# Kernel optimization log

Hardware: AMD Instinct MI355X
Metric: run time of the kernel (lower is better)

Reference implementation:

```python
import jax, jax.numpy as jnp
import numpy as np

B, T, N, D, H, C = 32, 64, 22, 512, 8, 128
DEPTH = D // H


def setup_inputs() -> dict:
    key = jax.random.key(0)
    ks = jax.random.split(key, 10)
    s = 0.02
    return {
        "x": jax.random.normal(ks[0], (B, T, N, D), jnp.float32),
        "context": jax.random.normal(ks[1], (B, C, D), jnp.float32),
        "Wq": jax.random.normal(ks[2], (N, D, D), jnp.float32) * s,  # per-joint Q proj
        "bq": jax.random.normal(ks[3], (N, D), jnp.float32) * s,
        "Wk": jax.random.normal(ks[4], (D, D), jnp.float32) * s,
        "bk": jax.random.normal(ks[5], (D,), jnp.float32) * s,
        "Wv": jax.random.normal(ks[6], (D, D), jnp.float32) * s,
        "bv": jax.random.normal(ks[7], (D,), jnp.float32) * s,
        "Wout": jax.random.normal(ks[8], (D, D), jnp.float32) * s,
        "bout": jax.random.normal(ks[9], (D,), jnp.float32) * s,
    }


def reference(x, context, Wq, bq, Wk, bk, Wv, bv, Wout, bout):
    b, t, n, d = x.shape
    c = context.shape[1]
    h, dh = H, DEPTH
    # Per-joint Q projection fused into one batched GEMM: [B,T,N,D] x [N,D,D] -> [B,T,N,D]
    q = jnp.einsum('btnd,ndf->btnf', x, Wq) + bq  # bq broadcasts over (B,T)
    # Shared K/V computed ONCE (original recomputes per joint; math identical)
    k = context @ Wk + bk  # [B,C,D]
    v = context @ Wv + bv  # [B,C,D]
    # Split heads
    qh = q.reshape(b, t, n, h, dh)
    kh = k.reshape(b, c, h, dh)
    vh = v.reshape(b, c, h, dh)
    scale = 1.0 / float(np.sqrt(dh))
    # Attention logits per joint: [B,N,H,T,C]
    logits = jnp.einsum('btnhd,bchd->bnhtc', qh, kh) * scale
    attn = jax.nn.softmax(logits, axis=-1)
    # Attend shared V, merge heads: [B,T,N,D]
    o = jnp.einsum('bnhtc,bchd->btnhd', attn, vh).reshape(b, t, n, d)
    # Shared output projection
    return o @ Wout + bout
```

## Files before the change

### kernel.cpp

```cpp
#include <hip/hip_runtime.h>
#include <hip/hip_bf16.h>

#define NB 32
#define NT 64
#define NJ 22
#define ND 512
#define NH 8
#define NC 128
#define NDH 64
#define NR 1408

typedef __attribute__((ext_vector_type(8))) short s16x8;
typedef __attribute__((ext_vector_type(4))) float fx4;

static __device__ __forceinline__ unsigned short f2bf(float f) {
    unsigned u = __builtin_bit_cast(unsigned, f);
    u += 0x7fffu + ((u >> 16) & 1u);
    return (unsigned short)(u >> 16);
}

static __device__ __forceinline__ fx4 mfma16(s16x8 a, s16x8 b, fx4 c) {
    return __builtin_amdgcn_mfma_f32_16x16x32_bf16(a, b, c, 0, 0, 0);
}

static __device__ __forceinline__ void gload16(const void* g, void* l) {
    __builtin_amdgcn_global_load_lds(
        (const __attribute__((address_space(1))) void*)g,
        (__attribute__((address_space(3))) void*)l,
        16, 0, 0);
}

__global__ __launch_bounds__(256) void convswz_all_k(
    const float* __restrict__ x, const float* __restrict__ ctx,
    unsigned short* __restrict__ xbf, unsigned short* __restrict__ cbf)
{
    const long bid = blockIdx.x;
    const float* src; unsigned short* dst; long i; int key;
    if (bid < 11264) {
        i = (bid * 256 + threadIdx.x) * 8;
        src = x; dst = xbf;
        key = (int)(((unsigned)(i >> 9) / 22u) & 7u);
    } else {
        i = ((bid - 11264) * 256 + threadIdx.x) * 8;
        src = ctx; dst = cbf;
        key = (int)(((unsigned)(i >> 9)) & 7u);
    }
    const int c = (int)((i >> 3) & 7);
    const long j = (i & ~63L) | ((long)(c ^ key) << 3);
    const float4 a = *reinterpret_cast<const float4*>(src + i);
    const float4 b = *reinterpret_cast<const float4*>(src + i + 4);
    unsigned short t[8];
    t[0]=f2bf(a.x); t[1]=f2bf(a.y); t[2]=f2bf(a.z); t[3]=f2bf(a.w);
    t[4]=f2bf(b.x); t[5]=f2bf(b.y); t[6]=f2bf(b.z); t[7]=f2bf(b.w);
    *reinterpret_cast<s16x8*>(dst + j) = *reinterpret_cast<s16x8*>(t);
}

__global__ __launch_bounds__(256) void twconv_all_k(
    const float* __restrict__ Wq, const float* __restrict__ Wk,
    const float* __restrict__ Wv, const float* __restrict__ Wout,
    unsigned short* __restrict__ WqT, unsigned short* __restrict__ WkT,
    unsigned short* __restrict__ WvT, unsigned short* __restrict__ WoutT)
{
    __shared__ float T[64][65];
    const int z = blockIdx.z;
    const float* W; unsigned short* Wt;
    if (z < 22)       { W = Wq + (long)z * 262144; Wt = WqT + (long)z * 262144; }
    else if (z == 22) { W = Wk;   Wt = WkT; }
    else if (z == 23) { W = Wv;   Wt = WvT; }
    else              { W = Wout; Wt = WoutT; }

    const int tid = threadIdx.x;
    W  += (long)blockIdx.x * 64 * 512 + blockIdx.y * 64;
    Wt += (long)blockIdx.y * 64 * 512 + blockIdx.x * 64;
    const int r = tid >> 2, c0 = (tid & 3) * 16;
    #pragma unroll
    for (int i = 0; i < 4; ++i) {
        const float4 p = *reinterpret_cast<const float4*>(W + (long)r * 512 + c0 + i*4);
        T[r][c0 + i*4 + 0] = p.x; T[r][c0 + i*4 + 1] = p.y;
        T[r][c0 + i*4 + 2] = p.z; T[r][c0 + i*4 + 3] = p.w;
    }
    __syncthreads();
    unsigned short o[16];
    #pragma unroll
    for (int i = 0; i < 16; ++i) o[i] = f2bf(T[c0 + i][r]);
    const int ch0 = ((c0 >> 3) ^ (r & 7));
    *reinterpret_cast<s16x8*>(Wt + (long)r * 512 + ch0*8)     = *reinterpret_cast<s16x8*>(o);
    *reinterpret_cast<s16x8*>(Wt + (long)r * 512 + (ch0^1)*8) = *reinterpret_cast<s16x8*>(o + 8);
}

template <typename TC, int MODE>
__global__ __launch_bounds__(256) void gemm128_k(
    const unsigned short* __restrict__ A, long lda,
    const unsigned short* __restrict__ Bt,
    const float* __restrict__ bias,
    TC* __restrict__ C, long ldc,
    long jsA, long jsW, long jsB, long jsC,
    const unsigned short* __restrict__ Bt2,
    const float* __restrict__ bias2,
    TC* __restrict__ C2)
{
    __shared__ unsigned short As[2][128*64];
    __shared__ unsigned short Bs[2][128*64];

    const int tid = threadIdx.x;
    const int w = tid >> 6, lane = tid & 63;
    const long j = blockIdx.z;

    const int nx = gridDim.x;
    const int nwg = nx * gridDim.y;
    int lin = blockIdx.y * nx + blockIdx.x;
    lin = (lin & 7) * (nwg >> 3) + (lin >> 3);
    const int bx = lin % nx, by = lin / nx;

    int kv = 0;
    int byv = by;
    if constexpr (MODE == 3) {
        if (by >= 4) { kv = 2; byv = by - 4; Bt = Bt2; bias = bias2; C = C2; }
        else         { kv = 1; }
    }

    A    += (long)bx * 128 * lda + j * jsA;
    Bt   += j * jsW + (long)byv * 128 * 512;
    bias += j * jsB + byv * 128;
    if constexpr (MODE == 0)
        C += (long)bx * 128 * ldc + j * jsC + byv * 128;

    const int srow = lane >> 3;
    const int scol = (lane & 7) * 8;
    const unsigned short* Ag = A  + (long)(w*8 + srow) * lda + scol;
    const unsigned short* Bg = Bt + (long)(w*8 + srow) * 512 + scol;

    const int lr = lane & 15, lk = lane >> 4;
    const int wm = w >> 1, wn = w & 1;

    fx4 acc[4][4] = {};

    auto STAGE = [&](int buf, int kt) {
        char* Al = (char*)&As[buf][0] + w * 1024;
        char* Bl = (char*)&Bs[buf][0] + w * 1024;
        #pragma unroll
        for (int it = 0; it < 4; ++it)
            gload16(Ag + (long)it * 32 * lda + kt, Al + it * 4096);
        #pragma unroll
        for (int it = 0; it < 4; ++it)
            gload16(Bg + (long)it * 32 * 512 + kt, Bl + it * 4096);
    };

    auto COMPUTE = [&](int buf) {
        #pragma unroll
        for (int ks = 0; ks < 2; ++ks) {
            const int cha = (ks*4 + lk) ^ (lr & 7);
            s16x8 a[4], b[4];
            #pragma unroll
            for (int m = 0; m < 4; ++m)
                a[m] = *reinterpret_cast<const s16x8*>(&As[buf][(wm*64 + m*16 + lr)*64 + cha*8]);
            #pragma unroll
            for (int n = 0; n < 4; ++n)
                b[n] = *reinterpret_cast<const s16x8*>(&Bs[buf][(wn*64 + n*16 + lr)*64 + cha*8]);
            #pragma unroll
            for (int m = 0; m < 4; ++m)
                #pragma unroll
                for (int n = 0; n < 4; ++n)
                    acc[m][n] = mfma16(a[m], b[n], acc[m][n]);
        }
    };

    STAGE(0, 0);
    __syncthreads();
    #pragma unroll
    for (int t = 0; t < 7; ++t) {
        const int cur = t & 1;
        STAGE(cur ^ 1, (t + 1) * 64);
        COMPUTE(cur);
        __syncthreads();
    }
    COMPUTE(1);

    #pragma unroll
    for (int n = 0; n < 4; ++n) {
        const int col = wn*64 + n*16 + lr;
        const float bv = bias[col];
        #pragma unroll
        for (int m = 0; m < 4; ++m) {
            #pragma unroll
            for (int r = 0; r < 4; ++r) {
                const int row = wm*64 + m*16 + lk*4 + r;
                const float val = acc[m][n][r] + bv;
                if constexpr (MODE == 0) {
                    if constexpr (sizeof(TC) == 2)
                        reinterpret_cast<unsigned short*>(C)[(long)row*ldc + col] = f2bf(val);
                    else
                        reinterpret_cast<float*>(C)[(long)row*ldc + col] = val;
                } else {
                    const int grow = bx*128 + row;
                    const int gcol = byv*128 + col;
                    const int b = grow >> 7, c = grow & 127;
                    const int hh = gcol >> 6, dh = gcol & 63;
                    unsigned short* Cp = reinterpret_cast<unsigned short*>(C);
                    if (kv == 1) {
                        const int dhs = (dh & 7) | ((((dh >> 3) ^ (c & 7)) & 7) << 3);
                        Cp[(((long)b*8 + hh)*128 + c)*64 + dhs] = f2bf(val);
                    } else {
                        const int cs = (c & 7) | ((((c >> 3) ^ (dh & 7)) & 15) << 3);
                        Cp[(((long)b*8 + hh)*64 + dh)*128 + cs] = f2bf(val);
                    }
                }
            }
        }
    }
}

__global__ __launch_bounds__(256, 4) void attn3_k(
    const unsigned short* __restrict__ q,
    const unsigned short* __restrict__ kt,
    const unsigned short* __restrict__ vt,
    unsigned short* __restrict__ o)
{
    __shared__ __align__(16) unsigned short smem[20480];
    unsigned short* Qs = smem;
    unsigned short* Ks = smem + 4096;
    unsigned short* Vs = smem + 12288;

    const int tid = threadIdx.x;
    const int w = tid >> 6, lane = tid & 63;
    const int lr = lane & 15, lk = lane >> 4;
    const int r0 = blockIdx.x * 64;
    const int h = blockIdx.y;
    const int b = blockIdx.z;

    const unsigned short* qg = q + ((long)b*NR + r0 + w*16 + (lane>>3))*512
                                 + h*64 + (lane & 7)*8;
    const unsigned short* kg = kt + ((long)(b*8+h))*8192 + w*2048 + lane*8;
    const unsigned short* vg = vt + ((long)(b*8+h))*8192 + w*2048 + lane*8;

    gload16(qg,            (char*)Qs + w*2048);
    gload16(qg + 8*512,    (char*)Qs + w*2048 + 1024);
    #pragma unroll
    for (int it = 0; it < 4; ++it) {
        gload16(kg + it*512, (char*)Ks + w*4096 + it*1024);
        gload16(vg + it*512, (char*)Vs + w*4096 + it*1024);
    }
    __syncthreads();

    s16x8 aq[2];
    #pragma unroll
    for (int kk = 0; kk < 2; ++kk)
        aq[kk] = *reinterpret_cast<const s16x8*>(&Qs[(w*16 + lr)*64 + kk*32 + lk*8]);

    fx4 s[8] = {};
    __builtin_amdgcn_s_setprio(1);
    #pragma unroll
    for (int kk = 0; kk < 2; ++kk) {
        #pragma unroll
        for (int f = 0; f < 8; ++f) {
            const int c = f*16 + lr;
            const int chunk = (kk*4 + lk) ^ (c & 7);
            s16x8 bk = *reinterpret_cast<const s16x8*>(&Ks[c*64 + chunk*8]);
            s[f] = mfma16(aq[kk], bk, s[f]);
        }
    }
    __builtin_amdgcn_s_setprio(0);
    __syncthreads();

    unsigned short* P = Ks;

    const float SC = 0.125f * 1.44269504088896340736f;
    #pragma unroll
    for (int rr = 0; rr < 4; ++rr) {
        const int row = w*16 + lk*4 + rr;
        float mx = -3.0e38f;
        #pragma unroll
        for (int f = 0; f < 8; ++f) mx = fmaxf(mx, s[f][rr]);
        #pragma unroll
        for (int off = 1; off < 16; off <<= 1) mx = fmaxf(mx, __shfl_xor(mx, off));
        float p[8]; float sum = 0.f;
        #pragma unroll
        for (int f = 0; f < 8; ++f) {
            p[f] = exp2f((s[f][rr] - mx) * SC);
            sum += p[f];
        }
        #pragma unroll
        for (int off = 1; off < 16; off <<= 1) sum += __shfl_xor(sum, off);
        const float inv = 1.0f / sum;
        #pragma unroll
        for (int f = 0; f < 8; ++f) {
            const int cg = f*16 + lr;
            P[row*128 + (((cg >> 3) ^ (row & 7)) << 3) + (cg & 7)] = f2bf(p[f] * inv);
        }
    }

    fx4 oacc[4] = {};
    __builtin_amdgcn_s_setprio(1);
    #pragma unroll
    for (int kt4 = 0; kt4 < 4; ++kt4) {
        const int prow = w*16 + lr;
        s16x8 ap = *reinterpret_cast<const s16x8*>(
            &P[prow*128 + (((kt4*4 + lk) ^ (prow & 7)) << 3)]);
        #pragma unroll
        for (int bn = 0; bn < 4; ++bn) {
            const int dh = bn*16 + lr;
            const int chunk = (kt4*4 + lk) ^ (dh & 7);
            s16x8 bv = *reinterpret_cast<const s16x8*>(&Vs[dh*128 + chunk*8]);
            oacc[bn] = mfma16(ap, bv, oacc[bn]);
        }
    }
    __builtin_amdgcn_s_setprio(0);

    unsigned short* ob = o + ((long)b*NR + r0)*512 + h*64;
    #pragma unroll
    for (int bn = 0; bn < 4; ++bn)
        #pragma unroll
        for (int rr = 0; rr < 4; ++rr) {
            const int row = w*16 + lk*4 + rr;
            const int colg = bn*16 + lr;
            const int ch = ((colg >> 3) ^ (row & 7));
            ob[(long)row*512 + ch*8 + (lr & 7)] = f2bf(oacc[bn][rr]);
        }
}

extern "C" void kernel_launch(void* const* d_in, const int* in_sizes, int n_in,
                              void* d_out, int out_size, void* d_ws, size_t ws_size,
                              hipStream_t stream)
{
    const float* x    = (const float*)d_in[0];
    const float* ctx  = (const float*)d_in[1];
    const float* Wq   = (const float*)d_in[2];
    const float* bq   = (const float*)d_in[3];
    const float* Wk   = (const float*)d_in[4];
    const float* bk   = (const float*)d_in[5];
    const float* Wv   = (const float*)d_in[6];
    const float* bv   = (const float*)d_in[7];
    const float* Wout = (const float*)d_in[8];
    const float* bout = (const float*)d_in[9];
    float* out = (float*)d_out;

    const size_t NX  = (size_t)45056 * 512;
    const size_t NKV = (size_t)4096 * 512;
    const size_t NW  = (size_t)512 * 512;

    unsigned short* xbf   = (unsigned short*)d_ws;
    unsigned short* qbf   = xbf   + NX;
    unsigned short* cbf   = qbf   + NX;
    unsigned short* ktp   = cbf   + NKV;
    unsigned short* vtp   = ktp   + NKV;
    unsigned short* WqT   = vtp   + NKV;
    unsigned short* WkT   = WqT   + 22 * NW;
    unsigned short* WvT   = WkT   + NW;
    unsigned short* WoutT = WvT   + NW;
    unsigned short* obf   = xbf;

    convswz_all_k<<<dim3(12288), 256, 0, stream>>>(x, ctx, xbf, cbf);
    twconv_all_k<<<dim3(8, 8, 25), 256, 0, stream>>>(
        Wq, Wk, Wv, Wout, WqT, WkT, WvT, WoutT);

    gemm128_k<unsigned short, 0><<<dim3(16, 4, NJ), 256, 0, stream>>>(
        xbf, (long)NJ*ND, WqT, bq, qbf, (long)NJ*ND,
        (long)ND, (long)NW, (long)ND, (long)ND,
        nullptr, nullptr, nullptr);

    gemm128_k<unsigned short, 3><<<dim3(32, 8, 1), 256, 0, stream>>>(
        cbf, ND, WkT, bk, ktp, ND, 0, 0, 0, 0,
        WvT, bv, vtp);

    attn3_k<<<dim3(NR/64, NH, NB), 256, 0, stream>>>(qbf, ktp, vtp, obf);

    gemm128_k<float, 0><<<dim3(45056/128, 4, 1), 256, 0, stream>>>(
        obf, ND, WoutT, bout, out, ND, 0, 0, 0, 0,
        nullptr, nullptr, nullptr);
}
```

Measured before the change: 189.0 us.

## Merge conversion kernels and process two query tiles per attention block

Folds the weight transpose/convert kernel into the activation convert kernel, so one launch handles both and one launch overhead disappears. The attention kernel now handles 128 query rows per block as two 64-row tiles, loading K and V into shared memory once for both. Q goes straight from global memory into registers instead of being staged through shared memory, and the softmax row reductions use DPP row-rotate ops instead of shuffles. In exchange, shared memory per block grows, the occupancy hint drops to 3, and there are half as many attention blocks.

```diff
diff --git a/kernel.cpp b/kernel.cpp
--- a/kernel.cpp
+++ b/kernel.cpp
@@ -30,62 +30,71 @@
         16, 0, 0);
 }
 
-__global__ __launch_bounds__(256) void convswz_all_k(
+template <int CTRL>
+static __device__ __forceinline__ float ror16(float v) {
+    return __builtin_bit_cast(float,
+        __builtin_amdgcn_update_dpp(0, __builtin_bit_cast(int, v),
+                                    CTRL, 0xf, 0xf, true));
+}
+
+__global__ __launch_bounds__(256) void conv_all_k(
     const float* __restrict__ x, const float* __restrict__ ctx,
-    unsigned short* __restrict__ xbf, unsigned short* __restrict__ cbf)
+    const float* __restrict__ Wq, const float* __restrict__ Wk,
+    const float* __restrict__ Wv, const float* __restrict__ Wout,
+    unsigned short* __restrict__ xbf, unsigned short* __restrict__ cbf,
+    unsigned short* __restrict__ WqT, unsigned short* __restrict__ WkT,
+    unsigned short* __restrict__ WvT, unsigned short* __restrict__ WoutT)
 {
+    __shared__ float T[64][65];
     const long bid = blockIdx.x;
+    const int tid = threadIdx.x;
+
+    if (bid < 1600) {
+        const int z = (int)(bid >> 6);
+        const int rem = (int)(bid & 63);
+        const int tbx = rem >> 3, tby = rem & 7;
+        const float* W; unsigned short* Wt;
+        if (z < 22)       { W = Wq + (long)z * 262144; Wt = WqT + (long)z * 262144; }
+        else if (z == 22) { W = Wk;   Wt = WkT; }
+        else if (z == 23) { W = Wv;   Wt = WvT; }
+        else              { W = Wout; Wt = WoutT; }
+        W  += (long)tbx * 64 * 512 + tby * 64;
+        Wt += (long)tby * 64 * 512 + tbx * 64;
+        const int r = tid >> 2, c0 = (tid & 3) * 16;
+        #pragma unroll
+        for (int i = 0; i < 4; ++i) {
+            const float4 p = *reinterpret_cast<const float4*>(W + (long)r * 512 + c0 + i*4);
+            T[r][c0 + i*4 + 0] = p.x; T[r][c0 + i*4 + 1] = p.y;
+            T[r][c0 + i*4 + 2] = p.z; T[r][c0 + i*4 + 3] = p.w;
+        }
+        __syncthreads();
+        unsigned short o[16];
+        #pragma unroll
+        for (int i = 0; i < 16; ++i) o[i] = f2bf(T[c0 + i][r]);
+        const int ch0 = ((c0 >> 3) ^ (r & 7));
+        *reinterpret_cast<s16x8*>(Wt + (long)r * 512 + ch0*8)     = *reinterpret_cast<s16x8*>(o);
+        *reinterpret_cast<s16x8*>(Wt + (long)r * 512 + (ch0^1)*8) = *reinterpret_cast<s16x8*>(o + 8);
+        return;
+    }
+
     const float* src; unsigned short* dst; long i; int key;
-    if (bid < 11264) {
-        i = (bid * 256 + threadIdx.x) * 8;
+    if (bid < 2624) {
+        i = ((bid - 1600) * 256 + tid) * 8;
+        src = ctx; dst = cbf;
+        key = (int)(((unsigned)(i >> 9)) & 7u);
+    } else {
+        i = ((bid - 2624) * 256 + tid) * 8;
         src = x; dst = xbf;
         key = (int)(((unsigned)(i >> 9) / 22u) & 7u);
-    } else {
-        i = ((bid - 11264) * 256 + threadIdx.x) * 8;
-        src = ctx; dst = cbf;
-        key = (int)(((unsigned)(i >> 9)) & 7u);
     }
     const int c = (int)((i >> 3) & 7);
-    const long j = (i & ~63L) | ((long)(c ^ key) << 3);
+    const long jj = (i & ~63L) | ((long)(c ^ key) << 3);
     const float4 a = *reinterpret_cast<const float4*>(src + i);
     const float4 b = *reinterpret_cast<const float4*>(src + i + 4);
     unsigned short t[8];
     t[0]=f2bf(a.x); t[1]=f2bf(a.y); t[2]=f2bf(a.z); t[3]=f2bf(a.w);
     t[4]=f2bf(b.x); t[5]=f2bf(b.y); t[6]=f2bf(b.z); t[7]=f2bf(b.w);
-    *reinterpret_cast<s16x8*>(dst + j) = *reinterpret_cast<s16x8*>(t);
-}
-
-__global__ __launch_bounds__(256) void twconv_all_k(
-    const float* __restrict__ Wq, const float* __restrict__ Wk,
-    const float* __restrict__ Wv, const float* __restrict__ Wout,
-    unsigned short* __restrict__ WqT, unsigned short* __restrict__ WkT,
-    unsigned short* __restrict__ WvT, unsigned short* __restrict__ WoutT)
-{
-    __shared__ float T[64][65];
-    const int z = blockIdx.z;
-    const float* W; unsigned short* Wt;
-    if (z < 22)       { W = Wq + (long)z * 262144; Wt = WqT + (long)z * 262144; }
-    else if (z == 22) { W = Wk;   Wt = WkT; }
-    else if (z == 23) { W = Wv;   Wt = WvT; }
-    else              { W = Wout; Wt = WoutT; }
-
-    const int tid = threadIdx.x;
-    W  += (long)blockIdx.x * 64 * 512 + blockIdx.y * 64;
-    Wt += (long)blockIdx.y * 64 * 512 + blockIdx.x * 64;
-    const int r = tid >> 2, c0 = (tid & 3) * 16;
-    #pragma unroll
-    for (int i = 0; i < 4; ++i) {
-        const float4 p = *reinterpret_cast<const float4*>(W + (long)r * 512 + c0 + i*4);
-        T[r][c0 + i*4 + 0] = p.x; T[r][c0 + i*4 + 1] = p.y;
-        T[r][c0 + i*4 + 2] = p.z; T[r][c0 + i*4 + 3] = p.w;
-    }
-    __syncthreads();
-    unsigned short o[16];
-    #pragma unroll
-    for (int i = 0; i < 16; ++i) o[i] = f2bf(T[c0 + i][r]);
-    const int ch0 = ((c0 >> 3) ^ (r & 7));
-    *reinterpret_cast<s16x8*>(Wt + (long)r * 512 + ch0*8)     = *reinterpret_cast<s16x8*>(o);
-    *reinterpret_cast<s16x8*>(Wt + (long)r * 512 + (ch0^1)*8) = *reinterpret_cast<s16x8*>(o + 8);
+    *reinterpret_cast<s16x8*>(dst + jj) = *reinterpret_cast<s16x8*>(t);
 }
 
 template <typename TC, int MODE>
@@ -210,112 +219,114 @@
     }
 }
 
-__global__ __launch_bounds__(256, 4) void attn3_k(
+__global__ __launch_bounds__(256, 3) void attn4_k(
     const unsigned short* __restrict__ q,
     const unsigned short* __restrict__ kt,
     const unsigned short* __restrict__ vt,
     unsigned short* __restrict__ o)
 {
-    __shared__ __align__(16) unsigned short smem[20480];
-    unsigned short* Qs = smem;
-    unsigned short* Ks = smem + 4096;
-    unsigned short* Vs = smem + 12288;
+    __shared__ __align__(16) unsigned short Ks[128*64];
+    __shared__ __align__(16) unsigned short Vs[64*128];
+    __shared__ __align__(16) unsigned short Ps[64*128];
 
     const int tid = threadIdx.x;
     const int w = tid >> 6, lane = tid & 63;
     const int lr = lane & 15, lk = lane >> 4;
-    const int r0 = blockIdx.x * 64;
+    const int r0 = blockIdx.x * 128;
     const int h = blockIdx.y;
     const int b = blockIdx.z;
 
-    const unsigned short* qg = q + ((long)b*NR + r0 + w*16 + (lane>>3))*512
-                                 + h*64 + (lane & 7)*8;
     const unsigned short* kg = kt + ((long)(b*8+h))*8192 + w*2048 + lane*8;
     const unsigned short* vg = vt + ((long)(b*8+h))*8192 + w*2048 + lane*8;
-
-    gload16(qg,            (char*)Qs + w*2048);
-    gload16(qg + 8*512,    (char*)Qs + w*2048 + 1024);
     #pragma unroll
     for (int it = 0; it < 4; ++it) {
         gload16(kg + it*512, (char*)Ks + w*4096 + it*1024);
         gload16(vg + it*512, (char*)Vs + w*4096 + it*1024);
     }
+
+    s16x8 qr[2][2];
+    #pragma unroll
+    for (int t = 0; t < 2; ++t) {
+        const unsigned short* qb = q + ((long)b*NR + r0 + t*64 + w*16 + lr)*512 + h*64;
+        #pragma unroll
+        for (int kk = 0; kk < 2; ++kk)
+            qr[t][kk] = *reinterpret_cast<const s16x8*>(qb + kk*32 + lk*8);
+    }
     __syncthreads();
 
-    s16x8 aq[2];
-    #pragma unroll
-    for (int kk = 0; kk < 2; ++kk)
-        aq[kk] = *reinterpret_cast<const s16x8*>(&Qs[(w*16 + lr)*64 + kk*32 + lk*8]);
-
-    fx4 s[8] = {};
-    __builtin_amdgcn_s_setprio(1);
-    #pragma unroll
-    for (int kk = 0; kk < 2; ++kk) {
-        #pragma unroll
-        for (int f = 0; f < 8; ++f) {
-            const int c = f*16 + lr;
-            const int chunk = (kk*4 + lk) ^ (c & 7);
-            s16x8 bk = *reinterpret_cast<const s16x8*>(&Ks[c*64 + chunk*8]);
-            s[f] = mfma16(aq[kk], bk, s[f]);
-        }
-    }
-    __builtin_amdgcn_s_setprio(0);
-    __syncthreads();
-
-    unsigned short* P = Ks;
-
     const float SC = 0.125f * 1.44269504088896340736f;
-    #pragma unroll
-    for (int rr = 0; rr < 4; ++rr) {
-        const int row = w*16 + lk*4 + rr;
-        float mx = -3.0e38f;
-        #pragma unroll
-        for (int f = 0; f < 8; ++f) mx = fmaxf(mx, s[f][rr]);
-        #pragma unroll
-        for (int off = 1; off < 16; off <<= 1) mx = fmaxf(mx, __shfl_xor(mx, off));
-        float p[8]; float sum = 0.f;
-        #pragma unroll
-        for (int f = 0; f < 8; ++f) {
-            p[f] = exp2f((s[f][rr] - mx) * SC);
-            sum += p[f];
-        }
-        #pragma unroll
-        for (int off = 1; off < 16; off <<= 1) sum += __shfl_xor(sum, off);
-        const float inv = 1.0f / sum;
-        #pragma unroll
-        for (int f = 0; f < 8; ++f) {
-            const int cg = f*16 + lr;
-            P[row*128 + (((cg >> 3) ^ (row & 7)) << 3) + (cg & 7)] = f2bf(p[f] * inv);
-        }
-    }
-
-    fx4 oacc[4] = {};
-    __builtin_amdgcn_s_setprio(1);
-    #pragma unroll
-    for (int kt4 = 0; kt4 < 4; ++kt4) {
-        const int prow = w*16 + lr;
-        s16x8 ap = *reinterpret_cast<const s16x8*>(
-            &P[prow*128 + (((kt4*4 + lk) ^ (prow & 7)) << 3)]);
-        #pragma unroll
-        for (int bn = 0; bn < 4; ++bn) {
-            const int dh = bn*16 + lr;
-            const int chunk = (kt4*4 + lk) ^ (dh & 7);
-            s16x8 bv = *reinterpret_cast<const s16x8*>(&Vs[dh*128 + chunk*8]);
-            oacc[bn] = mfma16(ap, bv, oacc[bn]);
-        }
-    }
-    __builtin_amdgcn_s_setprio(0);
-
-    unsigned short* ob = o + ((long)b*NR + r0)*512 + h*64;
-    #pragma unroll
-    for (int bn = 0; bn < 4; ++bn)
+
+    #pragma unroll
+    for (int t = 0; t < 2; ++t) {
+        fx4 s[8] = {};
+        __builtin_amdgcn_s_setprio(1);
+        #pragma unroll
+        for (int kk = 0; kk < 2; ++kk) {
+            #pragma unroll
+            for (int f = 0; f < 8; ++f) {
+                const int c = f*16 + lr;
+                const int chunk = (kk*4 + lk) ^ (c & 7);
+                s16x8 bk = *reinterpret_cast<const s16x8*>(&Ks[c*64 + chunk*8]);
+                s[f] = mfma16(qr[t][kk], bk, s[f]);
+            }
+        }
+        __builtin_amdgcn_s_setprio(0);
+
         #pragma unroll
         for (int rr = 0; rr < 4; ++rr) {
             const int row = w*16 + lk*4 + rr;
-            const int colg = bn*16 + lr;
-            const int ch = ((colg >> 3) ^ (row & 7));
-            ob[(long)row*512 + ch*8 + (lr & 7)] = f2bf(oacc[bn][rr]);
-        }
+            float mx = fmaxf(fmaxf(fmaxf(s[0][rr], s[1][rr]), fmaxf(s[2][rr], s[3][rr])),
+                             fmaxf(fmaxf(s[4][rr], s[5][rr]), fmaxf(s[6][rr], s[7][rr])));
+            mx = fmaxf(mx, ror16<0x128>(mx));
+            mx = fmaxf(mx, ror16<0x124>(mx));
+            mx = fmaxf(mx, ror16<0x122>(mx));
+            mx = fmaxf(mx, ror16<0x121>(mx));
+            float p[8]; float sum = 0.f;
+            #pragma unroll
+            for (int f = 0; f < 8; ++f) {
+                p[f] = exp2f((s[f][rr] - mx) * SC);
+                sum += p[f];
+            }
+            sum += ror16<0x128>(sum);
+            sum += ror16<0x124>(sum);
+            sum += ror16<0x122>(sum);
+            sum += ror16<0x121>(sum);
+            const float inv = 1.0f / sum;
+            #pragma unroll
+            for (int f = 0; f < 8; ++f) {
+                const int cg = f*16 + lr;
+                Ps[row*128 + (((cg >> 3) ^ (row & 7)) << 3) + (cg & 7)] = f2bf(p[f] * inv);
+            }
+        }
+
+        fx4 oacc[4] = {};
+        __builtin_amdgcn_s_setprio(1);
+        #pragma unroll
+        for (int kt4 = 0; kt4 < 4; ++kt4) {
+            const int prow = w*16 + lr;
+            s16x8 ap = *reinterpret_cast<const s16x8*>(
+                &Ps[prow*128 + (((kt4*4 + lk) ^ (prow & 7)) << 3)]);
+            #pragma unroll
+            for (int bn = 0; bn < 4; ++bn) {
+                const int dh = bn*16 + lr;
+                const int chunk = (kt4*4 + lk) ^ (dh & 7);
+                s16x8 bv = *reinterpret_cast<const s16x8*>(&Vs[dh*128 + chunk*8]);
+                oacc[bn] = mfma16(ap, bv, oacc[bn]);
+            }
+        }
+        __builtin_amdgcn_s_setprio(0);
+
+        unsigned short* ob = o + ((long)b*NR + r0 + t*64)*512 + h*64;
+        #pragma unroll
+        for (int bn = 0; bn < 4; ++bn)
+            #pragma unroll
+            for (int rr = 0; rr < 4; ++rr) {
+                const int row = w*16 + lk*4 + rr;
+                const int colg = bn*16 + lr;
+                const int ch = ((colg >> 3) ^ (row & 7));
+                ob[(long)row*512 + ch*8 + (lr & 7)] = f2bf(oacc[bn][rr]);
+            }
+    }
 }
 
 extern "C" void kernel_launch(void* const* d_in, const int* in_sizes, int n_in,
@@ -349,9 +360,8 @@
     unsigned short* WoutT = WvT   + NW;
     unsigned short* obf   = xbf;
 
-    convswz_all_k<<<dim3(12288), 256, 0, stream>>>(x, ctx, xbf, cbf);
-    twconv_all_k<<<dim3(8, 8, 25), 256, 0, stream>>>(
-        Wq, Wk, Wv, Wout, WqT, WkT, WvT, WoutT);
+    conv_all_k<<<dim3(13888), 256, 0, stream>>>(
+        x, ctx, Wq, Wk, Wv, Wout, xbf, cbf, WqT, WkT, WvT, WoutT);
 
     gemm128_k<unsigned short, 0><<<dim3(16, 4, NJ), 256, 0, stream>>>(
         xbf, (long)NJ*ND, WqT, bq, qbf, (long)NJ*ND,
@@ -362,7 +372,7 @@
         cbf, ND, WkT, bk, ktp, ND, 0, 0, 0, 0,
         WvT, bv, vtp);
 
-    attn3_k<<<dim3(NR/64, NH, NB), 256, 0, stream>>>(qbf, ktp, vtp, obf);
+    attn4_k<<<dim3(NR/128, NH, NB), 256, 0, stream>>>(qbf, ktp, vtp, obf);
 
     gemm128_k<float, 0><<<dim3(45056/128, 4, 1), 256, 0, stream>>>(
         obf, ND, WoutT, bout, out, ND, 0, 0, 0, 0,
```

Measured after the change: 182.4 us. 3.5% less time.
